# Performance work log

Measured on AMD Instinct MI355X. Metric: run time of the kernel, lower is better.

Reference implementation:

```python
import jax, jax.numpy as jnp
import numpy as np

SINKHORN_ITERS = 5
EPS = 1e-12  # torch F.normalize eps


def _l2norm(x):
    n = jnp.sqrt(jnp.sum(x * x, axis=-1, keepdims=True))
    return x / jnp.maximum(n, EPS)


def setup_inputs() -> dict:
    key = jax.random.key(0)
    k1, k2, k3, k4 = jax.random.split(key, 4)
    B, Nd, Ns, D, Dm = 8, 2048, 2048, 1024, 256
    drone_nodes = jax.random.normal(k1, (B, Nd, D), dtype=jnp.float32)
    sat_nodes = jax.random.normal(k2, (B, Ns, D), dtype=jnp.float32)
    # match_proj parameters (nn.Linear(d_model, match_dim))
    lim = 1.0 / np.sqrt(D)
    W = jax.random.uniform(k3, (D, Dm), minval=-lim, maxval=lim, dtype=jnp.float32)
    b = jax.random.uniform(k4, (Dm,), minval=-lim, maxval=lim, dtype=jnp.float32)
    return {"drone_nodes": drone_nodes, "sat_nodes": sat_nodes, "W": W, "b": b}


def reference(drone_nodes, sat_nodes, W, b):
    # project + L2-normalize each node embedding
    d = _l2norm(drone_nodes @ W + b)   # [B, Nd, Dm]
    s = _l2norm(sat_nodes @ W + b)     # [B, Ns, Dm]
    M0 = jnp.einsum('bnd,bmd->bnm', d, s)  # [B, Nd, Ns] cosine similarities
    M = M0
    for _ in range(SINKHORN_ITERS):
        M = M - jax.nn.logsumexp(M, axis=2, keepdims=True)
        M = M - jax.nn.logsumexp(M, axis=1, keepdims=True)
    assignment = jnp.exp(M)
    denom = min(d.shape[1], s.shape[1])
    match_score = jnp.sum(assignment * M0, axis=(1, 2)) / denom  # [B]
    return (assignment, match_score)
```

## Files before the change

kernel.cpp:

```cpp
#include <hip/hip_runtime.h>
#include <math.h>

#define BATCH 8
#define NNODE 2048
#define DIN   1024
#define DM    256
#define ROWS_TOTAL (BATCH * NNODE)

typedef unsigned short u16;
typedef __attribute__((ext_vector_type(8))) short short8;
typedef __attribute__((ext_vector_type(4))) float f32x4;

__device__ __forceinline__ u16 f2b(float f) {
    union { float f; unsigned u; } v; v.f = f;
    unsigned r = v.u + 0x7fffu + ((v.u >> 16) & 1u);
    return (u16)(r >> 16);
}
__device__ __forceinline__ float b2f(u16 h) {
    union { unsigned u; float f; } v; v.u = ((unsigned)h) << 16; return v.f;
}

template <typename MT> struct Ld8;
template <> struct Ld8<u16> {
    static __device__ __forceinline__ void go(const u16* p, float* x) {
        short8 r = *(const short8*)p;
        #pragma unroll
        for (int j = 0; j < 8; ++j) x[j] = b2f((u16)r[j]);
    }
};
template <> struct Ld8<float> {
    static __device__ __forceinline__ void go(const float* p, float* x) {
        float4 a = *(const float4*)p, b = *(const float4*)(p + 4);
        x[0]=a.x; x[1]=a.y; x[2]=a.z; x[3]=a.w;
        x[4]=b.x; x[5]=b.y; x[6]=b.z; x[7]=b.w;
    }
};

__global__ __launch_bounds__(256) void cvgm_prep_w(
    const float* __restrict__ W, u16* __restrict__ Wt)
{
    __shared__ float t[32][33];
    const int tx = threadIdx.x & 31, ty = threadIdx.x >> 5;
    const int k0 = blockIdx.x * 32, c0 = blockIdx.y * 32;
    #pragma unroll
    for (int r = 0; r < 4; ++r) {
        const int kl = ty * 4 + r;
        t[kl][tx] = W[(size_t)(k0 + kl) * DM + c0 + tx];
    }
    __syncthreads();
    #pragma unroll
    for (int r = 0; r < 4; ++r) {
        const int cl = ty * 4 + r;
        Wt[(size_t)(c0 + cl) * DIN + k0 + tx] = f2b(t[tx][cl]);
    }
}

__global__ __launch_bounds__(256) void cvgm_proj_mfma(
    const float* __restrict__ X, const u16* __restrict__ Wt,
    const float* __restrict__ bias, u16* __restrict__ P)
{
    __shared__ u16 As[32 * 64];
    __shared__ u16 Bs[256 * 64];
    __shared__ float rsum[4][32];

    const int tid = threadIdx.x;
    const int lane = tid & 63, wid = tid >> 6;
    const int l15 = lane & 15, l4 = lane >> 4;
    const int row0 = blockIdx.x * 32;

    f32x4 acc[2][4];
    #pragma unroll
    for (int m = 0; m < 2; ++m)
        #pragma unroll
        for (int n = 0; n < 4; ++n) acc[m][n] = (f32x4){0.f, 0.f, 0.f, 0.f};

    const int arow = tid >> 3, ac = tid & 7;

    for (int k0 = 0; k0 < DIN; k0 += 64) {
        const float* src = X + (size_t)(row0 + arow) * DIN + k0 + ac * 8;
        const float4 x0 = *(const float4*)src;
        const float4 x1 = *(const float4*)(src + 4);
        short8 wb[8];
        #pragma unroll
        for (int it = 0; it < 8; ++it) {
            const int id = it * 256 + tid;
            const int col = id >> 3, cc = id & 7;
            wb[it] = *(const short8*)(Wt + (size_t)col * DIN + k0 + cc * 8);
        }
        __syncthreads();
        short8 ap;
        ap[0]=(short)f2b(x0.x); ap[1]=(short)f2b(x0.y); ap[2]=(short)f2b(x0.z); ap[3]=(short)f2b(x0.w);
        ap[4]=(short)f2b(x1.x); ap[5]=(short)f2b(x1.y); ap[6]=(short)f2b(x1.z); ap[7]=(short)f2b(x1.w);
        *(short8*)(As + (arow * 8 + (ac ^ (arow & 7))) * 8) = ap;
        #pragma unroll
        for (int it = 0; it < 8; ++it) {
            const int id = it * 256 + tid;
            const int col = id >> 3, cc = id & 7;
            *(short8*)(Bs + (col * 8 + (cc ^ (col & 7))) * 8) = wb[it];
        }
        __syncthreads();
        #pragma unroll
        for (int ks = 0; ks < 2; ++ks) {
            const int ch = ks * 4 + l4;
            short8 af[2], bfr[4];
            #pragma unroll
            for (int m = 0; m < 2; ++m) {
                const int row = m * 16 + l15;
                af[m] = *(const short8*)(As + (row * 8 + (ch ^ (row & 7))) * 8);
            }
            #pragma unroll
            for (int n = 0; n < 4; ++n) {
                const int col = wid * 64 + n * 16 + l15;
                bfr[n] = *(const short8*)(Bs + (col * 8 + (ch ^ (col & 7))) * 8);
            }
            #pragma unroll
            for (int m = 0; m < 2; ++m)
                #pragma unroll
                for (int n = 0; n < 4; ++n)
                    acc[m][n] = __builtin_amdgcn_mfma_f32_16x16x32_bf16(af[m], bfr[n], acc[m][n], 0, 0, 0);
        }
        __syncthreads();
    }

    #pragma unroll
    for (int n = 0; n < 4; ++n) {
        const float bv = bias[wid * 64 + n * 16 + l15];
        #pragma unroll
        for (int m = 0; m < 2; ++m)
            #pragma unroll
            for (int r = 0; r < 4; ++r) acc[m][n][r] += bv;
    }
    float ss[2][4];
    #pragma unroll
    for (int m = 0; m < 2; ++m)
        #pragma unroll
        for (int r = 0; r < 4; ++r) {
            float s = 0.f;
            #pragma unroll
            for (int n = 0; n < 4; ++n) s += acc[m][n][r] * acc[m][n][r];
            s += __shfl_xor(s, 1); s += __shfl_xor(s, 2);
            s += __shfl_xor(s, 4); s += __shfl_xor(s, 8);
            ss[m][r] = s;
        }
    if (l15 == 0) {
        #pragma unroll
        for (int m = 0; m < 2; ++m)
            #pragma unroll
            for (int r = 0; r < 4; ++r) rsum[wid][m * 16 + l4 * 4 + r] = ss[m][r];
    }
    __syncthreads();
    #pragma unroll
    for (int m = 0; m < 2; ++m)
        #pragma unroll
        for (int r = 0; r < 4; ++r) {
            const int row = m * 16 + l4 * 4 + r;
            const float tot = rsum[0][row] + rsum[1][row] + rsum[2][row] + rsum[3][row];
            const float inv = 1.0f / fmaxf(sqrtf(tot), 1e-12f);
            #pragma unroll
            for (int n = 0; n < 4; ++n) {
                const int col = wid * 64 + n * 16 + l15;
                P[(size_t)(row0 + row) * DM + col] = f2b(acc[m][n][r] * inv);
            }
        }
}

template <typename OT>
__global__ __launch_bounds__(256) void cvgm_m0_mfma(
    const u16* __restrict__ Dp, const u16* __restrict__ Sp, OT* __restrict__ C)
{
    __shared__ u16 As[128 * 64];
    __shared__ u16 Bs[128 * 64];

    const int tid = threadIdx.x;
    const int lane = tid & 63, wid = tid >> 6;
    const int wr = wid >> 1, wc = wid & 1;
    const int l15 = lane & 15, l4 = lane >> 4;
    const int bb = blockIdx.z;
    const int i0 = blockIdx.y * 128, j0 = blockIdx.x * 128;
    const u16* Db = Dp + (size_t)bb * NNODE * DM;
    const u16* Sb = Sp + (size_t)bb * NNODE * DM;

    f32x4 acc[4][4];
    #pragma unroll
    for (int m = 0; m < 4; ++m)
        #pragma unroll
        for (int n = 0; n < 4; ++n) acc[m][n] = (f32x4){0.f, 0.f, 0.f, 0.f};

    for (int k0 = 0; k0 < DM; k0 += 64) {
        short8 ra[4], rb[4];
        #pragma unroll
        for (int it = 0; it < 4; ++it) {
            const int id = it * 256 + tid;
            const int row = id >> 3, c = id & 7;
            ra[it] = *(const short8*)(Db + (size_t)(i0 + row) * DM + k0 + c * 8);
            rb[it] = *(const short8*)(Sb + (size_t)(j0 + row) * DM + k0 + c * 8);
        }
        __syncthreads();
        #pragma unroll
        for (int it = 0; it < 4; ++it) {
            const int id = it * 256 + tid;
            const int row = id >> 3, c = id & 7;
            const int sl = row * 8 + (c ^ (row & 7));
            *(short8*)(As + sl * 8) = ra[it];
            *(short8*)(Bs + sl * 8) = rb[it];
        }
        __syncthreads();
        #pragma unroll
        for (int ks = 0; ks < 2; ++ks) {
            const int ch = ks * 4 + l4;
            short8 af[4], bfr[4];
            #pragma unroll
            for (int m = 0; m < 4; ++m) {
                const int row = wr * 64 + m * 16 + l15;
                af[m] = *(const short8*)(As + (row * 8 + (ch ^ (row & 7))) * 8);
            }
            #pragma unroll
            for (int n = 0; n < 4; ++n) {
                const int col = wc * 64 + n * 16 + l15;
                bfr[n] = *(const short8*)(Bs + (col * 8 + (ch ^ (col & 7))) * 8);
            }
            #pragma unroll
            for (int m = 0; m < 4; ++m)
                #pragma unroll
                for (int n = 0; n < 4; ++n)
                    acc[m][n] = __builtin_amdgcn_mfma_f32_16x16x32_bf16(af[m], bfr[n], acc[m][n], 0, 0, 0);
        }
        __syncthreads();
    }

    OT* Cb = C + (size_t)bb * NNODE * NNODE;
    #pragma unroll
    for (int m = 0; m < 4; ++m) {
        const int row = i0 + wr * 64 + m * 16 + l4 * 4;
        #pragma unroll
        for (int n = 0; n < 4; ++n) {
            const int col = j0 + wc * 64 + n * 16 + l15;
            #pragma unroll
            for (int r = 0; r < 4; ++r) {
                const float val = acc[m][n][r];
                if constexpr (sizeof(OT) == 2)
                    Cb[(size_t)(row + r) * NNODE + col] = (OT)f2b(val);
                else
                    Cb[(size_t)(row + r) * NNODE + col] = (OT)val;
            }
        }
    }
}

template <typename MT>
__global__ __launch_bounds__(256) void cvgm_row_lse(
    const MT* __restrict__ M0, const float* __restrict__ v, float* __restrict__ u)
{
    const int row = blockIdx.x;
    const int b = row >> 11;
    const MT* Mr = M0 + (size_t)row * NNODE;
    const float* vb = v + (b << 11);
    const int j0 = threadIdx.x * 8;

    float x[8];
    Ld8<MT>::go(Mr + j0, x);
    const float4 va = *(const float4*)(vb + j0);
    const float4 vc = *(const float4*)(vb + j0 + 4);
    const float vv[8] = {va.x, va.y, va.z, va.w, vc.x, vc.y, vc.z, vc.w};
    float s = 0.f;
    #pragma unroll
    for (int k = 0; k < 8; ++k) s += __expf(x[k] - vv[k]);
    #pragma unroll
    for (int off = 1; off < 64; off <<= 1) s += __shfl_xor(s, off);
    __shared__ float sh[4];
    if ((threadIdx.x & 63) == 0) sh[threadIdx.x >> 6] = s;
    __syncthreads();
    if (threadIdx.x == 0) u[row] = __logf(sh[0] + sh[1] + sh[2] + sh[3]);
}

template <typename MT>
__global__ __launch_bounds__(256) void cvgm_col_part(
    const MT* __restrict__ M0, const float* __restrict__ u, float* __restrict__ ps)
{
    const int chunk = blockIdx.x;
    const int b = blockIdx.y;
    const int j0 = threadIdx.x * 8;
    const MT* Mb = M0 + ((size_t)(b << 11) + chunk * 32) * NNODE;
    const float* ub = u + (b << 11) + chunk * 32;

    float s[8] = {0.f, 0.f, 0.f, 0.f, 0.f, 0.f, 0.f, 0.f};
    for (int i = 0; i < 32; ++i) {
        const float ui = ub[i];
        float x[8];
        Ld8<MT>::go(Mb + (size_t)i * NNODE + j0, x);
        #pragma unroll
        for (int c = 0; c < 8; ++c) s[c] += __expf(x[c] - ui);
    }
    float* dst = ps + (size_t)(b * 64 + chunk) * NNODE + j0;
    *(float4*)(dst)     = make_float4(s[0], s[1], s[2], s[3]);
    *(float4*)(dst + 4) = make_float4(s[4], s[5], s[6], s[7]);
}

__global__ __launch_bounds__(256) void cvgm_col_merge(
    const float* __restrict__ ps, float* __restrict__ v)
{
    const int idx = blockIdx.x * 256 + threadIdx.x;
    const int b = idx >> 11, j = idx & 2047;
    float s = 0.f;
    #pragma unroll 8
    for (int c = 0; c < 64; ++c) s += ps[(size_t)(b * 64 + c) * NNODE + j];
    v[idx] = __logf(s);
}

template <typename MT>
__global__ __launch_bounds__(256) void cvgm_final(
    const MT* M0, const float* __restrict__ u, const float* __restrict__ v,
    float* out, float* __restrict__ spart)
{
    const int row = blockIdx.x;
    const int b = row >> 11;
    const MT* Mr = M0 + (size_t)row * NNODE;
    float* Or = out + (size_t)row * NNODE;
    const float* vb = v + (b << 11);
    const float ui = u[row];
    const int j0 = threadIdx.x * 8;

    float x[8];
    Ld8<MT>::go(Mr + j0, x);
    const float4 va = *(const float4*)(vb + j0);
    const float4 vc = *(const float4*)(vb + j0 + 4);
    const float vv[8] = {va.x, va.y, va.z, va.w, vc.x, vc.y, vc.z, vc.w};
    float a[8], accv = 0.f;
    #pragma unroll
    for (int k = 0; k < 8; ++k) {
        a[k] = __expf(x[k] - ui - vv[k]);
        accv += a[k] * x[k];
    }
    *(float4*)(Or + j0)     = make_float4(a[0], a[1], a[2], a[3]);
    *(float4*)(Or + j0 + 4) = make_float4(a[4], a[5], a[6], a[7]);

    #pragma unroll
    for (int off = 1; off < 64; off <<= 1) accv += __shfl_xor(accv, off);
    __shared__ float sh[4];
    if ((threadIdx.x & 63) == 0) sh[threadIdx.x >> 6] = accv;
    __syncthreads();
    if (threadIdx.x == 0) spart[row] = sh[0] + sh[1] + sh[2] + sh[3];
}

__global__ __launch_bounds__(256) void cvgm_score(
    const float* __restrict__ spart, float* __restrict__ score)
{
    const int b = blockIdx.x;
    float acc = 0.f;
    for (int t = threadIdx.x; t < NNODE; t += 256) acc += spart[(b << 11) + t];
    #pragma unroll
    for (int off = 1; off < 64; off <<= 1) acc += __shfl_xor(acc, off);
    __shared__ float sh[4];
    if ((threadIdx.x & 63) == 0) sh[threadIdx.x >> 6] = acc;
    __syncthreads();
    if (threadIdx.x == 0) score[b] = (sh[0] + sh[1] + sh[2] + sh[3]) * (1.0f / 2048.0f);
}

extern "C" void kernel_launch(void* const* d_in, const int* in_sizes, int n_in,
                              void* d_out, int out_size, void* d_ws, size_t ws_size,
                              hipStream_t stream) {
    (void)in_sizes; (void)n_in; (void)out_size;
    const float* drone = (const float*)d_in[0];
    const float* sat   = (const float*)d_in[1];
    const float* W     = (const float*)d_in[2];
    const float* bias  = (const float*)d_in[3];

    float* out   = (float*)d_out;
    float* score = out + (size_t)BATCH * NNODE * NNODE;

    char* ws = (char*)d_ws;
    const size_t SZ_M0B  = (size_t)BATCH * NNODE * NNODE * 2;
    const size_t SZ_PROJ = (size_t)ROWS_TOTAL * DM * 2;
    const size_t SZ_WT   = (size_t)DM * DIN * 2;
    const size_t SZ_UV   = (size_t)ROWS_TOTAL * 4;
    const size_t SZ_PS   = (size_t)BATCH * 64 * NNODE * 4;
    const size_t NEED_BIG = SZ_M0B + 2 * SZ_PROJ + SZ_WT + 3 * SZ_UV + SZ_PS;

    const bool big = ws_size >= NEED_BIG;

    if (big) {
        u16* M0b   = (u16*)ws;
        u16* dproj = (u16*)(ws + SZ_M0B);
        u16* sproj = dproj + (size_t)ROWS_TOTAL * DM;
        u16* Wt    = sproj + (size_t)ROWS_TOTAL * DM;
        float* u   = (float*)(ws + SZ_M0B + 2 * SZ_PROJ + SZ_WT);
        float* v   = u + ROWS_TOTAL;
        float* ps  = v + ROWS_TOTAL;
        float* spart = ps + (size_t)BATCH * 64 * NNODE;

        hipMemsetAsync(v, 0, SZ_UV, stream);
        cvgm_prep_w<<<dim3(32, 8), 256, 0, stream>>>(W, Wt);
        cvgm_proj_mfma<<<ROWS_TOTAL / 32, 256, 0, stream>>>(drone, Wt, bias, dproj);
        cvgm_proj_mfma<<<ROWS_TOTAL / 32, 256, 0, stream>>>(sat, Wt, bias, sproj);
        cvgm_m0_mfma<u16><<<dim3(16, 16, 8), 256, 0, stream>>>(dproj, sproj, M0b);
        for (int it = 0; it < 5; ++it) {
            cvgm_row_lse<u16><<<ROWS_TOTAL, 256, 0, stream>>>(M0b, v, u);
            cvgm_col_part<u16><<<dim3(64, 8), 256, 0, stream>>>(M0b, u, ps);
            cvgm_col_merge<<<ROWS_TOTAL / 256, 256, 0, stream>>>(ps, v);
        }
        cvgm_final<u16><<<ROWS_TOTAL, 256, 0, stream>>>(M0b, u, v, out, spart);
        cvgm_score<<<BATCH, 256, 0, stream>>>(spart, score);
    } else {
        float* M0  = out;
        u16* dproj = (u16*)ws;
        u16* sproj = dproj + (size_t)ROWS_TOTAL * DM;
        u16* Wt    = sproj + (size_t)ROWS_TOTAL * DM;
        float* u   = (float*)(ws + 2 * SZ_PROJ + SZ_WT);
        float* v   = u + ROWS_TOTAL;
        float* ps  = v + ROWS_TOTAL;
        float* spart = ps + (size_t)BATCH * 64 * NNODE;

        hipMemsetAsync(v, 0, SZ_UV, stream);
        cvgm_prep_w<<<dim3(32, 8), 256, 0, stream>>>(W, Wt);
        cvgm_proj_mfma<<<ROWS_TOTAL / 32, 256, 0, stream>>>(drone, Wt, bias, dproj);
        cvgm_proj_mfma<<<ROWS_TOTAL / 32, 256, 0, stream>>>(sat, Wt, bias, sproj);
        cvgm_m0_mfma<float><<<dim3(16, 16, 8), 256, 0, stream>>>(dproj, sproj, M0);
        for (int it = 0; it < 5; ++it) {
            cvgm_row_lse<float><<<ROWS_TOTAL, 256, 0, stream>>>(M0, v, u);
            cvgm_col_part<float><<<dim3(64, 8), 256, 0, stream>>>(M0, u, ps);
            cvgm_col_merge<<<ROWS_TOTAL / 256, 256, 0, stream>>>(ps, v);
        }
        cvgm_final<float><<<ROWS_TOTAL, 256, 0, stream>>>(M0, u, v, out, spart);
        cvgm_score<<<BATCH, 256, 0, stream>>>(spart, score);
    }
}
```

Baseline: 283.1 us.

## Quantize M0 to int8 and fuse row/column Sinkhorn passes into one kernel

Writes an int8-quantized copy of the cosine matrix alongside bf16 and runs each Sinkhorn iteration as one fused kernel. That kernel stages a row stripe in LDS, computes row log-sum-exps, then accumulates column partial sums from the same stripe, all in base-2 exp/log. The drone and sat projections are merged into one 512-thread launch, and the final pass is restructured to process 32 rows per block. The aim is to cut the repeated full-matrix reads per iteration, at the cost of int8 quantization error (about 1/127 in logits) in the Sinkhorn normalizers.

```diff
diff --git a/kernel.cpp b/kernel.cpp
--- a/kernel.cpp
+++ b/kernel.cpp
@@ -7,6 +7,9 @@
 #define DM    256
 #define ROWS_TOTAL (BATCH * NNODE)
 
+#define LOG2E 1.4426950408889634f
+#define Q127  0.011359803471566641f
+
 typedef unsigned short u16;
 typedef __attribute__((ext_vector_type(8))) short short8;
 typedef __attribute__((ext_vector_type(4))) float f32x4;
@@ -19,22 +22,9 @@
 __device__ __forceinline__ float b2f(u16 h) {
     union { unsigned u; float f; } v; v.u = ((unsigned)h) << 16; return v.f;
 }
-
-template <typename MT> struct Ld8;
-template <> struct Ld8<u16> {
-    static __device__ __forceinline__ void go(const u16* p, float* x) {
-        short8 r = *(const short8*)p;
-        #pragma unroll
-        for (int j = 0; j < 8; ++j) x[j] = b2f((u16)r[j]);
-    }
-};
-template <> struct Ld8<float> {
-    static __device__ __forceinline__ void go(const float* p, float* x) {
-        float4 a = *(const float4*)p, b = *(const float4*)(p + 4);
-        x[0]=a.x; x[1]=a.y; x[2]=a.z; x[3]=a.w;
-        x[4]=b.x; x[5]=b.y; x[6]=b.z; x[7]=b.w;
-    }
-};
+__device__ __forceinline__ float dqi(unsigned wd, int k) {
+    return (float)((int)(wd << ((3 - k) * 8)) >> 24);
+}
 
 __global__ __launch_bounds__(256) void cvgm_prep_w(
     const float* __restrict__ W, u16* __restrict__ Wt)
@@ -55,18 +45,23 @@
     }
 }
 
-__global__ __launch_bounds__(256) void cvgm_proj_mfma(
-    const float* __restrict__ X, const u16* __restrict__ Wt,
-    const float* __restrict__ bias, u16* __restrict__ P)
-{
-    __shared__ u16 As[32 * 64];
+__global__ __launch_bounds__(512) void cvgm_proj_mfma(
+    const float* __restrict__ Xd, const float* __restrict__ Xs,
+    const u16* __restrict__ Wt, const float* __restrict__ bias,
+    u16* __restrict__ Pd, u16* __restrict__ Ps)
+{
+    __shared__ u16 As[64 * 64];
     __shared__ u16 Bs[256 * 64];
-    __shared__ float rsum[4][32];
+    __shared__ float rsum[4][64];
+
+    const float* X = blockIdx.y ? Xs : Xd;
+    u16* P = blockIdx.y ? Ps : Pd;
 
     const int tid = threadIdx.x;
     const int lane = tid & 63, wid = tid >> 6;
+    const int wr = wid >> 2, wc = wid & 3;
     const int l15 = lane & 15, l4 = lane >> 4;
-    const int row0 = blockIdx.x * 32;
+    const int row0 = blockIdx.x * 64;
 
     f32x4 acc[2][4];
     #pragma unroll
@@ -80,10 +75,10 @@
         const float* src = X + (size_t)(row0 + arow) * DIN + k0 + ac * 8;
         const float4 x0 = *(const float4*)src;
         const float4 x1 = *(const float4*)(src + 4);
-        short8 wb[8];
-        #pragma unroll
-        for (int it = 0; it < 8; ++it) {
-            const int id = it * 256 + tid;
+        short8 wb[4];
+        #pragma unroll
+        for (int it = 0; it < 4; ++it) {
+            const int id = it * 512 + tid;
             const int col = id >> 3, cc = id & 7;
             wb[it] = *(const short8*)(Wt + (size_t)col * DIN + k0 + cc * 8);
         }
@@ -93,8 +88,8 @@
         ap[4]=(short)f2b(x1.x); ap[5]=(short)f2b(x1.y); ap[6]=(short)f2b(x1.z); ap[7]=(short)f2b(x1.w);
         *(short8*)(As + (arow * 8 + (ac ^ (arow & 7))) * 8) = ap;
         #pragma unroll
-        for (int it = 0; it < 8; ++it) {
-            const int id = it * 256 + tid;
+        for (int it = 0; it < 4; ++it) {
+            const int id = it * 512 + tid;
             const int col = id >> 3, cc = id & 7;
             *(short8*)(Bs + (col * 8 + (cc ^ (col & 7))) * 8) = wb[it];
         }
@@ -105,12 +100,12 @@
             short8 af[2], bfr[4];
             #pragma unroll
             for (int m = 0; m < 2; ++m) {
-                const int row = m * 16 + l15;
+                const int row = wr * 32 + m * 16 + l15;
                 af[m] = *(const short8*)(As + (row * 8 + (ch ^ (row & 7))) * 8);
             }
             #pragma unroll
             for (int n = 0; n < 4; ++n) {
-                const int col = wid * 64 + n * 16 + l15;
+                const int col = wc * 64 + n * 16 + l15;
                 bfr[n] = *(const short8*)(Bs + (col * 8 + (ch ^ (col & 7))) * 8);
             }
             #pragma unroll
@@ -124,13 +119,12 @@
 
     #pragma unroll
     for (int n = 0; n < 4; ++n) {
-        const float bv = bias[wid * 64 + n * 16 + l15];
+        const float bv = bias[wc * 64 + n * 16 + l15];
         #pragma unroll
         for (int m = 0; m < 2; ++m)
             #pragma unroll
             for (int r = 0; r < 4; ++r) acc[m][n][r] += bv;
     }
-    float ss[2][4];
     #pragma unroll
     for (int m = 0; m < 2; ++m)
         #pragma unroll
@@ -140,33 +134,28 @@
             for (int n = 0; n < 4; ++n) s += acc[m][n][r] * acc[m][n][r];
             s += __shfl_xor(s, 1); s += __shfl_xor(s, 2);
             s += __shfl_xor(s, 4); s += __shfl_xor(s, 8);
-            ss[m][r] = s;
-        }
-    if (l15 == 0) {
-        #pragma unroll
-        for (int m = 0; m < 2; ++m)
-            #pragma unroll
-            for (int r = 0; r < 4; ++r) rsum[wid][m * 16 + l4 * 4 + r] = ss[m][r];
-    }
+            if (l15 == 0) rsum[wc][wr * 32 + m * 16 + l4 * 4 + r] = s;
+        }
     __syncthreads();
     #pragma unroll
     for (int m = 0; m < 2; ++m)
         #pragma unroll
         for (int r = 0; r < 4; ++r) {
-            const int row = m * 16 + l4 * 4 + r;
+            const int row = wr * 32 + m * 16 + l4 * 4 + r;
             const float tot = rsum[0][row] + rsum[1][row] + rsum[2][row] + rsum[3][row];
             const float inv = 1.0f / fmaxf(sqrtf(tot), 1e-12f);
             #pragma unroll
             for (int n = 0; n < 4; ++n) {
-                const int col = wid * 64 + n * 16 + l15;
+                const int col = wc * 64 + n * 16 + l15;
                 P[(size_t)(row0 + row) * DM + col] = f2b(acc[m][n][r] * inv);
             }
         }
 }
 
-template <typename OT>
+template <int WQ>
 __global__ __launch_bounds__(256) void cvgm_m0_mfma(
-    const u16* __restrict__ Dp, const u16* __restrict__ Sp, OT* __restrict__ C)
+    const u16* __restrict__ Dp, const u16* __restrict__ Sp,
+    u16* __restrict__ C, char* __restrict__ Cq)
 {
     __shared__ u16 As[128 * 64];
     __shared__ u16 Bs[128 * 64];
@@ -228,7 +217,8 @@
         __syncthreads();
     }
 
-    OT* Cb = C + (size_t)bb * NNODE * NNODE;
+    u16* Cb = C + (size_t)bb * NNODE * NNODE;
+    char* Cqb = Cq + (size_t)bb * NNODE * NNODE;
     #pragma unroll
     for (int m = 0; m < 4; ++m) {
         const int row = i0 + wr * 64 + m * 16 + l4 * 4;
@@ -238,108 +228,181 @@
             #pragma unroll
             for (int r = 0; r < 4; ++r) {
                 const float val = acc[m][n][r];
-                if constexpr (sizeof(OT) == 2)
-                    Cb[(size_t)(row + r) * NNODE + col] = (OT)f2b(val);
-                else
-                    Cb[(size_t)(row + r) * NNODE + col] = (OT)val;
-            }
-        }
-    }
-}
-
-template <typename MT>
-__global__ __launch_bounds__(256) void cvgm_row_lse(
-    const MT* __restrict__ M0, const float* __restrict__ v, float* __restrict__ u)
-{
-    const int row = blockIdx.x;
-    const int b = row >> 11;
-    const MT* Mr = M0 + (size_t)row * NNODE;
-    const float* vb = v + (b << 11);
-    const int j0 = threadIdx.x * 8;
-
-    float x[8];
-    Ld8<MT>::go(Mr + j0, x);
-    const float4 va = *(const float4*)(vb + j0);
-    const float4 vc = *(const float4*)(vb + j0 + 4);
-    const float vv[8] = {va.x, va.y, va.z, va.w, vc.x, vc.y, vc.z, vc.w};
-    float s = 0.f;
-    #pragma unroll
-    for (int k = 0; k < 8; ++k) s += __expf(x[k] - vv[k]);
-    #pragma unroll
-    for (int off = 1; off < 64; off <<= 1) s += __shfl_xor(s, off);
-    __shared__ float sh[4];
-    if ((threadIdx.x & 63) == 0) sh[threadIdx.x >> 6] = s;
+                Cb[(size_t)(row + r) * NNODE + col] = f2b(val);
+                if constexpr (WQ) {
+                    int q = __float2int_rn(val * 127.f);
+                    q = q > 127 ? 127 : (q < -127 ? -127 : q);
+                    Cqb[(size_t)(row + r) * NNODE + col] = (char)q;
+                }
+            }
+        }
+    }
+}
+
+template <int ISQ>
+__global__ __launch_bounds__(256) void cvgm_rc(
+    const void* __restrict__ Mq_, const float* __restrict__ v2,
+    float* __restrict__ u2, float* __restrict__ ps)
+{
+    constexpr int RPC = ISQ ? 32 : 16;
+    constexpr int NCH = NNODE / RPC;
+    constexpr int RB  = ISQ ? NNODE : NNODE * 2;
+    __shared__ alignas(16) char stripe[RPC * RB];
+    __shared__ float u2s[RPC];
+
+    const int tid = threadIdx.x;
+    const int lane = tid & 63, w = tid >> 6;
+    const int b = blockIdx.y, chunk = blockIdx.x;
+    const size_t grow0 = ((size_t)b << 11) + chunk * RPC;
+
+    float vl[32];
+    const float* v2b = v2 + (b << 11);
+    #pragma unroll
+    for (int s = 0; s < 2; ++s)
+        #pragma unroll
+        for (int k = 0; k < 4; ++k)
+            *(float4*)(vl + s * 16 + k * 4) =
+                *(const float4*)(v2b + s * 1024 + lane * 16 + k * 4);
+
+    const char* gbase = (const char*)Mq_ + grow0 * RB;
+    constexpr int RW = RPC / 4;
+    #pragma unroll
+    for (int rr = 0; rr < RW; ++rr) {
+        const int r = w * RW + rr;
+        float s = 0.f;
+        if constexpr (ISQ) {
+            const char* rsrc = gbase + (size_t)r * RB;
+            #pragma unroll
+            for (int seg = 0; seg < 2; ++seg) {
+                const int4 d = *(const int4*)(rsrc + seg * 1024 + lane * 16);
+                *(int4*)(stripe + r * RB + seg * 1024 + lane * 16) = d;
+                const unsigned uu[4] = {(unsigned)d.x, (unsigned)d.y, (unsigned)d.z, (unsigned)d.w};
+                #pragma unroll
+                for (int q = 0; q < 4; ++q)
+                    #pragma unroll
+                    for (int k = 0; k < 4; ++k)
+                        s += exp2f(fmaf(dqi(uu[q], k), Q127, -vl[seg * 16 + q * 4 + k]));
+            }
+        } else {
+            const char* rsrc = gbase + (size_t)r * RB;
+            #pragma unroll
+            for (int seg = 0; seg < 2; ++seg) {
+                const int4 d0 = *(const int4*)(rsrc + seg * 2048 + lane * 32);
+                const int4 d1 = *(const int4*)(rsrc + seg * 2048 + lane * 32 + 16);
+                *(int4*)(stripe + r * RB + seg * 2048 + lane * 32) = d0;
+                *(int4*)(stripe + r * RB + seg * 2048 + lane * 32 + 16) = d1;
+                const unsigned uu[8] = {(unsigned)d0.x, (unsigned)d0.y, (unsigned)d0.z, (unsigned)d0.w,
+                                        (unsigned)d1.x, (unsigned)d1.y, (unsigned)d1.z, (unsigned)d1.w};
+                #pragma unroll
+                for (int q = 0; q < 8; ++q) {
+                    union { unsigned u; float f; } lo, hi;
+                    lo.u = uu[q] << 16; hi.u = uu[q] & 0xffff0000u;
+                    s += exp2f(fmaf(lo.f, LOG2E, -vl[seg * 16 + q * 2 + 0]));
+                    s += exp2f(fmaf(hi.f, LOG2E, -vl[seg * 16 + q * 2 + 1]));
+                }
+            }
+        }
+        #pragma unroll
+        for (int off = 1; off < 64; off <<= 1) s += __shfl_xor(s, off);
+        if (lane == 0) {
+            const float l2 = __log2f(s);
+            u2[grow0 + r] = l2;
+            u2s[r] = l2;
+        }
+    }
     __syncthreads();
-    if (threadIdx.x == 0) u[row] = __logf(sh[0] + sh[1] + sh[2] + sh[3]);
-}
-
-template <typename MT>
-__global__ __launch_bounds__(256) void cvgm_col_part(
-    const MT* __restrict__ M0, const float* __restrict__ u, float* __restrict__ ps)
-{
-    const int chunk = blockIdx.x;
-    const int b = blockIdx.y;
-    const int j0 = threadIdx.x * 8;
-    const MT* Mb = M0 + ((size_t)(b << 11) + chunk * 32) * NNODE;
-    const float* ub = u + (b << 11) + chunk * 32;
-
-    float s[8] = {0.f, 0.f, 0.f, 0.f, 0.f, 0.f, 0.f, 0.f};
-    for (int i = 0; i < 32; ++i) {
-        const float ui = ub[i];
-        float x[8];
-        Ld8<MT>::go(Mb + (size_t)i * NNODE + j0, x);
-        #pragma unroll
-        for (int c = 0; c < 8; ++c) s[c] += __expf(x[c] - ui);
-    }
-    float* dst = ps + (size_t)(b * 64 + chunk) * NNODE + j0;
-    *(float4*)(dst)     = make_float4(s[0], s[1], s[2], s[3]);
-    *(float4*)(dst + 4) = make_float4(s[4], s[5], s[6], s[7]);
-}
-
-__global__ __launch_bounds__(256) void cvgm_col_merge(
-    const float* __restrict__ ps, float* __restrict__ v)
+
+    const int j = tid * 8;
+    float sc[8] = {0.f, 0.f, 0.f, 0.f, 0.f, 0.f, 0.f, 0.f};
+    #pragma unroll 4
+    for (int i = 0; i < RPC; ++i) {
+        const float ui = u2s[i];
+        if constexpr (ISQ) {
+            const unsigned* pw = (const unsigned*)(stripe + i * RB + j);
+            const unsigned w0 = pw[0], w1 = pw[1];
+            #pragma unroll
+            for (int k = 0; k < 4; ++k) {
+                sc[k]     += exp2f(fmaf(dqi(w0, k), Q127, -ui));
+                sc[4 + k] += exp2f(fmaf(dqi(w1, k), Q127, -ui));
+            }
+        } else {
+            const unsigned* pw = (const unsigned*)(stripe + i * RB + j * 2);
+            #pragma unroll
+            for (int q = 0; q < 4; ++q) {
+                union { unsigned u; float f; } lo, hi;
+                lo.u = pw[q] << 16; hi.u = pw[q] & 0xffff0000u;
+                sc[q * 2 + 0] += exp2f(fmaf(lo.f, LOG2E, -ui));
+                sc[q * 2 + 1] += exp2f(fmaf(hi.f, LOG2E, -ui));
+            }
+        }
+    }
+    float* dst = ps + ((size_t)(b * NCH + chunk)) * NNODE + j;
+    *(float4*)(dst)     = make_float4(sc[0], sc[1], sc[2], sc[3]);
+    *(float4*)(dst + 4) = make_float4(sc[4], sc[5], sc[6], sc[7]);
+}
+
+__global__ __launch_bounds__(256) void cvgm_merge(
+    const float* __restrict__ ps, float* __restrict__ v2, int nch)
 {
     const int idx = blockIdx.x * 256 + threadIdx.x;
     const int b = idx >> 11, j = idx & 2047;
     float s = 0.f;
     #pragma unroll 8
-    for (int c = 0; c < 64; ++c) s += ps[(size_t)(b * 64 + c) * NNODE + j];
-    v[idx] = __logf(s);
-}
-
-template <typename MT>
+    for (int c = 0; c < nch; ++c) s += ps[(size_t)(b * nch + c) * NNODE + j];
+    v2[idx] = __log2f(s);
+}
+
 __global__ __launch_bounds__(256) void cvgm_final(
-    const MT* M0, const float* __restrict__ u, const float* __restrict__ v,
-    float* out, float* __restrict__ spart)
-{
-    const int row = blockIdx.x;
-    const int b = row >> 11;
-    const MT* Mr = M0 + (size_t)row * NNODE;
-    float* Or = out + (size_t)row * NNODE;
-    const float* vb = v + (b << 11);
-    const float ui = u[row];
-    const int j0 = threadIdx.x * 8;
-
-    float x[8];
-    Ld8<MT>::go(Mr + j0, x);
-    const float4 va = *(const float4*)(vb + j0);
-    const float4 vc = *(const float4*)(vb + j0 + 4);
-    const float vv[8] = {va.x, va.y, va.z, va.w, vc.x, vc.y, vc.z, vc.w};
-    float a[8], accv = 0.f;
-    #pragma unroll
-    for (int k = 0; k < 8; ++k) {
-        a[k] = __expf(x[k] - ui - vv[k]);
-        accv += a[k] * x[k];
-    }
-    *(float4*)(Or + j0)     = make_float4(a[0], a[1], a[2], a[3]);
-    *(float4*)(Or + j0 + 4) = make_float4(a[4], a[5], a[6], a[7]);
-
-    #pragma unroll
-    for (int off = 1; off < 64; off <<= 1) accv += __shfl_xor(accv, off);
-    __shared__ float sh[4];
-    if ((threadIdx.x & 63) == 0) sh[threadIdx.x >> 6] = accv;
-    __syncthreads();
-    if (threadIdx.x == 0) spart[row] = sh[0] + sh[1] + sh[2] + sh[3];
+    const u16* __restrict__ M0b, const float* __restrict__ u2,
+    const float* __restrict__ v2, float* __restrict__ out,
+    float* __restrict__ spart)
+{
+    const int tid = threadIdx.x;
+    const int lane = tid & 63, w = tid >> 6;
+    const int b = blockIdx.y, chunk = blockIdx.x;
+    const size_t grow0 = ((size_t)b << 11) + chunk * 32;
+
+    float vl[32];
+    const float* v2b = v2 + (b << 11);
+    #pragma unroll
+    for (int s = 0; s < 2; ++s)
+        #pragma unroll
+        for (int k = 0; k < 4; ++k)
+            *(float4*)(vl + s * 16 + k * 4) =
+                *(const float4*)(v2b + s * 1024 + lane * 16 + k * 4);
+
+    #pragma unroll
+    for (int rr = 0; rr < 8; ++rr) {
+        const size_t grow = grow0 + w * 8 + rr;
+        const float ui = u2[grow];
+        const char* rsrc = (const char*)(M0b + grow * NNODE);
+        float* drow = out + grow * NNODE;
+        float acc = 0.f;
+        #pragma unroll
+        for (int seg = 0; seg < 2; ++seg) {
+            const int4 d0 = *(const int4*)(rsrc + seg * 2048 + lane * 32);
+            const int4 d1 = *(const int4*)(rsrc + seg * 2048 + lane * 32 + 16);
+            const unsigned uu[8] = {(unsigned)d0.x, (unsigned)d0.y, (unsigned)d0.z, (unsigned)d0.w,
+                                    (unsigned)d1.x, (unsigned)d1.y, (unsigned)d1.z, (unsigned)d1.w};
+            float a[16];
+            #pragma unroll
+            for (int q = 0; q < 8; ++q) {
+                union { unsigned u; float f; } lo, hi;
+                lo.u = uu[q] << 16; hi.u = uu[q] & 0xffff0000u;
+                const float e0 = exp2f(fmaf(lo.f, LOG2E, -(ui + vl[seg * 16 + q * 2 + 0])));
+                const float e1 = exp2f(fmaf(hi.f, LOG2E, -(ui + vl[seg * 16 + q * 2 + 1])));
+                a[q * 2 + 0] = e0; a[q * 2 + 1] = e1;
+                acc += e0 * lo.f + e1 * hi.f;
+            }
+            float* dseg = drow + seg * 1024 + lane * 16;
+            #pragma unroll
+            for (int k = 0; k < 4; ++k)
+                *(float4*)(dseg + k * 4) = make_float4(a[k*4+0], a[k*4+1], a[k*4+2], a[k*4+3]);
+        }
+        #pragma unroll
+        for (int off = 1; off < 64; off <<= 1) acc += __shfl_xor(acc, off);
+        if (lane == 0) spart[grow] = acc;
+    }
 }
 
 __global__ __launch_bounds__(256) void cvgm_score(
@@ -370,57 +433,44 @@
 
     char* ws = (char*)d_ws;
     const size_t SZ_M0B  = (size_t)BATCH * NNODE * NNODE * 2;
+    const size_t SZ_M0Q  = (size_t)BATCH * NNODE * NNODE;
     const size_t SZ_PROJ = (size_t)ROWS_TOTAL * DM * 2;
     const size_t SZ_WT   = (size_t)DM * DIN * 2;
     const size_t SZ_UV   = (size_t)ROWS_TOTAL * 4;
-    const size_t SZ_PS   = (size_t)BATCH * 64 * NNODE * 4;
-    const size_t NEED_BIG = SZ_M0B + 2 * SZ_PROJ + SZ_WT + 3 * SZ_UV + SZ_PS;
-
-    const bool big = ws_size >= NEED_BIG;
-
-    if (big) {
-        u16* M0b   = (u16*)ws;
-        u16* dproj = (u16*)(ws + SZ_M0B);
-        u16* sproj = dproj + (size_t)ROWS_TOTAL * DM;
-        u16* Wt    = sproj + (size_t)ROWS_TOTAL * DM;
-        float* u   = (float*)(ws + SZ_M0B + 2 * SZ_PROJ + SZ_WT);
-        float* v   = u + ROWS_TOTAL;
-        float* ps  = v + ROWS_TOTAL;
-        float* spart = ps + (size_t)BATCH * 64 * NNODE;
-
-        hipMemsetAsync(v, 0, SZ_UV, stream);
-        cvgm_prep_w<<<dim3(32, 8), 256, 0, stream>>>(W, Wt);
-        cvgm_proj_mfma<<<ROWS_TOTAL / 32, 256, 0, stream>>>(drone, Wt, bias, dproj);
-        cvgm_proj_mfma<<<ROWS_TOTAL / 32, 256, 0, stream>>>(sat, Wt, bias, sproj);
-        cvgm_m0_mfma<u16><<<dim3(16, 16, 8), 256, 0, stream>>>(dproj, sproj, M0b);
+    const size_t SZ_PS   = (size_t)BATCH * 128 * NNODE * 4;
+
+    const size_t NEED_I8  = SZ_M0B + SZ_M0Q + 2 * SZ_PROJ + SZ_WT + 3 * SZ_UV + SZ_PS;
+    const bool use_i8 = ws_size >= NEED_I8;
+
+    size_t off = 0;
+    u16* M0b = (u16*)(ws + off); off += SZ_M0B;
+    char* M0q = (char*)(ws + off); if (use_i8) off += SZ_M0Q;
+    u16* dproj = (u16*)(ws + off); off += SZ_PROJ;
+    u16* sproj = (u16*)(ws + off); off += SZ_PROJ;
+    u16* Wt = (u16*)(ws + off); off += SZ_WT;
+    float* u2 = (float*)(ws + off); off += SZ_UV;
+    float* v2 = (float*)(ws + off); off += SZ_UV;
+    float* ps = (float*)(ws + off); off += SZ_PS;
+    float* spart = (float*)(ws + off);
+
+    hipMemsetAsync(v2, 0, SZ_UV, stream);
+    cvgm_prep_w<<<dim3(32, 8), 256, 0, stream>>>(W, Wt);
+    cvgm_proj_mfma<<<dim3(256, 2), 512, 0, stream>>>(drone, sat, Wt, bias, dproj, sproj);
+
+    if (use_i8) {
+        cvgm_m0_mfma<1><<<dim3(16, 16, 8), 256, 0, stream>>>(dproj, sproj, M0b, M0q);
         for (int it = 0; it < 5; ++it) {
-            cvgm_row_lse<u16><<<ROWS_TOTAL, 256, 0, stream>>>(M0b, v, u);
-            cvgm_col_part<u16><<<dim3(64, 8), 256, 0, stream>>>(M0b, u, ps);
-            cvgm_col_merge<<<ROWS_TOTAL / 256, 256, 0, stream>>>(ps, v);
-        }
-        cvgm_final<u16><<<ROWS_TOTAL, 256, 0, stream>>>(M0b, u, v, out, spart);
-        cvgm_score<<<BATCH, 256, 0, stream>>>(spart, score);
+            cvgm_rc<1><<<dim3(64, 8), 256, 0, stream>>>(M0q, v2, u2, ps);
+            cvgm_merge<<<ROWS_TOTAL / 256, 256, 0, stream>>>(ps, v2, 64);
+        }
     } else {
-        float* M0  = out;
-        u16* dproj = (u16*)ws;
-        u16* sproj = dproj + (size_t)ROWS_TOTAL * DM;
-        u16* Wt    = sproj + (size_t)ROWS_TOTAL * DM;
-        float* u   = (float*)(ws + 2 * SZ_PROJ + SZ_WT);
-        float* v   = u + ROWS_TOTAL;
-        float* ps  = v + ROWS_TOTAL;
-        float* spart = ps + (size_t)BATCH * 64 * NNODE;
-
-        hipMemsetAsync(v, 0, SZ_UV, stream);
-        cvgm_prep_w<<<dim3(32, 8), 256, 0, stream>>>(W, Wt);
-        cvgm_proj_mfma<<<ROWS_TOTAL / 32, 256, 0, stream>>>(drone, Wt, bias, dproj);
-        cvgm_proj_mfma<<<ROWS_TOTAL / 32, 256, 0, stream>>>(sat, Wt, bias, sproj);
-        cvgm_m0_mfma<float><<<dim3(16, 16, 8), 256, 0, stream>>>(dproj, sproj, M0);
+        cvgm_m0_mfma<0><<<dim3(16, 16, 8), 256, 0, stream>>>(dproj, sproj, M0b, M0q);
         for (int it = 0; it < 5; ++it) {
-            cvgm_row_lse<float><<<ROWS_TOTAL, 256, 0, stream>>>(M0, v, u);
-            cvgm_col_part<float><<<dim3(64, 8), 256, 0, stream>>>(M0, u, ps);
-            cvgm_col_merge<<<ROWS_TOTAL / 256, 256, 0, stream>>>(ps, v);
-        }
-        cvgm_final<float><<<ROWS_TOTAL, 256, 0, stream>>>(M0, u, v, out, spart);
-        cvgm_score<<<BATCH, 256, 0, stream>>>(spart, score);
-    }
-}
+            cvgm_rc<0><<<dim3(128, 8), 256, 0, stream>>>(M0b, v2, u2, ps);
+            cvgm_merge<<<ROWS_TOTAL / 256, 256, 0, stream>>>(ps, v2, 128);
+        }
+    }
+
+    cvgm_final<<<dim3(64, 8), 256, 0, stream>>>(M0b, u2, v2, out, spart);
+    cvgm_score<<<BATCH, 256, 0, stream>>>(spart, score);
+}
```

New measurement: 285.4 us. No clear change (+0.8%).
